# Kernel tuning notes

Measured on AMD Instinct MI355X. Metric: run time of the kernel, lower is better.

## Reference

```python
import jax, jax.numpy as jnp
import numpy as np

D_MODEL = 768
D_STATE = 16
D_CONV = 4
EXPAND = 2
N_LAYERS = 2
HEADDIM = 64
PATCH_DIM = 256
D_INNER = EXPAND * D_MODEL            # 1536
NHEADS = D_INNER // HEADDIM           # 24
CONV_DIM = D_INNER + 2 * D_STATE      # 1568 (x, B, C share the conv)
D_IN_PROJ = 2 * D_INNER + 2 * D_STATE + NHEADS  # 3128


def _mamba2(u, w_in, conv_w, conv_b, dt_bias, A_log, D, norm_w, w_out):
    """Mamba2 block (ngroups=1, rmsnorm=True, non-fused reference path)."""
    b, l, _ = u.shape
    zxbcdt = u @ w_in                                   # (b,l,D_IN_PROJ)
    z = zxbcdt[..., :D_INNER]
    xBC = zxbcdt[..., D_INNER:D_INNER + CONV_DIM]
    dt = jax.nn.softplus(zxbcdt[..., D_INNER + CONV_DIM:] + dt_bias)  # (b,l,H)
    # causal depthwise conv1d over L, then silu
    kernel = conv_w.T[:, None, :]                       # (D_CONV,1,CONV_DIM)
    xBC = jax.lax.conv_general_dilated(
        xBC, kernel, (1,), [(D_CONV - 1, 0)],
        dimension_numbers=('NLC', 'LIO', 'NLC'),
        feature_group_count=CONV_DIM) + conv_b
    xBC = jax.nn.silu(xBC)
    x = xBC[..., :D_INNER].reshape(b, l, NHEADS, HEADDIM)
    B = xBC[..., D_INNER:D_INNER + D_STATE]             # (b,l,N)
    C = xBC[..., D_INNER + D_STATE:]                    # (b,l,N)
    A = -jnp.exp(A_log)                                 # (H,)

    def step(h, inp):
        dt_t, x_t, b_t, c_t = inp                       # (b,H),(b,H,P),(b,N),(b,N)
        dA = jnp.exp(dt_t * A)                          # (b,H)
        h = h * dA[:, :, None, None] + jnp.einsum('bh,bhp,bn->bhpn', dt_t, x_t, b_t)
        y_t = jnp.einsum('bhpn,bn->bhp', h, c_t)
        return h, y_t

    h0 = jnp.zeros((b, NHEADS, HEADDIM, D_STATE), u.dtype)
    _, y = jax.lax.scan(step, h0,
                        (dt.swapaxes(0, 1), x.swapaxes(0, 1),
                         B.swapaxes(0, 1), C.swapaxes(0, 1)))
    y = y.swapaxes(0, 1) + x * D[:, None]               # skip: D per head
    y = y.reshape(b, l, D_INNER)
    # gated RMSNorm: rmsnorm(y * silu(z)) * weight
    g = y * jax.nn.silu(z)
    g = g * jax.lax.rsqrt(jnp.mean(g * g, axis=-1, keepdims=True) + 1e-5)
    y = g * norm_w
    return y @ w_out


def _backbone(patch_embeddings, Wp, bp, in_w, conv_w, conv_b, dt_bias,
              A_log, Dh, norm_w, out_w, bi_w, ls, fin_w):
    x = patch_embeddings @ Wp + bp
    for i in range(N_LAYERS):
        h_f = _mamba2(x, in_w[i, 0], conv_w[i, 0], conv_b[i, 0], dt_bias[i, 0],
                      A_log[i, 0], Dh[i, 0], norm_w[i, 0], out_w[i, 0])
        h_b = jnp.flip(_mamba2(jnp.flip(x, 1), in_w[i, 1], conv_w[i, 1],
                               conv_b[i, 1], dt_bias[i, 1], A_log[i, 1],
                               Dh[i, 1], norm_w[i, 1], out_w[i, 1]), 1)
        m = jnp.concatenate([h_f, h_b], axis=-1) @ bi_w[i]
        x = x + m * ls[i]
    # final RMSNorm with unit offset
    v = jnp.mean(x * x, axis=-1, keepdims=True)
    return x * jax.lax.rsqrt(v + 1e-6) * (1.0 + fin_w)


def setup_inputs() -> dict:
    key = jax.random.key(0)
    ks = jax.random.split(key, 14)
    L2 = (N_LAYERS, 2)
    pe = jax.random.normal(ks[0], (2, 2048, PATCH_DIM), jnp.float32)
    Wp = jax.random.normal(ks[1], (PATCH_DIM, D_MODEL), jnp.float32) * 0.02
    bp = jnp.zeros((D_MODEL,), jnp.float32)
    in_w = jax.random.normal(ks[2], L2 + (D_MODEL, D_IN_PROJ), jnp.float32) * 0.02
    conv_w = jax.random.normal(ks[3], L2 + (CONV_DIM, D_CONV), jnp.float32) * 0.2
    conv_b = jnp.zeros(L2 + (CONV_DIM,), jnp.float32)
    dt_bias = jax.random.uniform(ks[4], L2 + (NHEADS,), jnp.float32, -4.0, -2.0)
    A_log = jnp.log(jax.random.uniform(ks[5], L2 + (NHEADS,), jnp.float32, 1.0, 16.0))
    Dh = jax.random.normal(ks[6], L2 + (NHEADS,), jnp.float32) * 0.1 + 1.0
    norm_w = jnp.ones(L2 + (D_INNER,), jnp.float32)
    out_w = jax.random.normal(ks[7], L2 + (D_INNER, D_MODEL), jnp.float32) * 0.02
    bi_w = jax.random.normal(ks[8], (N_LAYERS, 2 * D_MODEL, D_MODEL), jnp.float32) * 0.02
    ls = jnp.full((N_LAYERS, D_MODEL), 1e-4, jnp.float32)
    fin_w = jnp.zeros((D_MODEL,), jnp.float32)
    return {"patch_embeddings": pe, "Wp": Wp, "bp": bp, "in_w": in_w,
            "conv_w": conv_w, "conv_b": conv_b, "dt_bias": dt_bias,
            "A_log": A_log, "Dh": Dh, "norm_w": norm_w, "out_w": out_w,
            "bi_w": bi_w, "ls": ls, "fin_w": fin_w}


def reference(patch_embeddings, Wp, bp, in_w, conv_w, conv_b, dt_bias,
              A_log, Dh, norm_w, out_w, bi_w, ls, fin_w):
    return _backbone(patch_embeddings, Wp, bp, in_w, conv_w, conv_b, dt_bias,
                     A_log, Dh, norm_w, out_w, bi_w, ls, fin_w)
```

## Files before the change

### kernel.cpp

```cpp
#include <hip/hip_runtime.h>

typedef unsigned short u16;
typedef short s16x8 __attribute__((ext_vector_type(8)));
typedef u16 u16x8 __attribute__((ext_vector_type(8)));
typedef float f32x4 __attribute__((ext_vector_type(4)));

__device__ inline float bf2f(u16 u) {
    union { unsigned int i; float f; } w; w.i = ((unsigned int)u) << 16; return w.f;
}
__device__ inline u16 f2bf(float f) {
    union { float f; unsigned int i; } w; w.f = f;
    unsigned int u = w.i;
    u += 0x7fffu + ((u >> 16) & 1u);
    return (u16)(u >> 16);
}

__global__ __launch_bounds__(256)
void wtransT(const float* __restrict__ src, u16* __restrict__ dst,
             int K, int N, int dstride, int src_z, int dz_hi, int dz_lo)
{
    int z = blockIdx.z;
    src += (size_t)z * src_z;
    dst += (size_t)(z >> 1) * dz_hi + (size_t)(z & 1) * dz_lo;
    __shared__ float t[32][33];
    int kt = blockIdx.y * 32, nt0 = blockIdx.x * 32;
    int lx = threadIdx.x & 31, ly = threadIdx.x >> 5;
#pragma unroll
    for (int i = 0; i < 32; i += 8) {
        int k = kt + ly + i, n = nt0 + lx;
        t[ly + i][lx] = (k < K && n < N) ? src[(size_t)k * N + n] : 0.f;
    }
    __syncthreads();
#pragma unroll
    for (int i = 0; i < 32; i += 8) {
        int n = nt0 + ly + i, k = kt + lx;
        if (n < N && k < K) dst[(size_t)n * dstride + k] = f2bf(t[lx][ly + i]);
    }
}

__global__ void cvtk(const float* __restrict__ src, u16* __restrict__ dst, int n) {
    int i = blockIdx.x * 256 + threadIdx.x;
    if (i < n) dst[i] = f2bf(src[i]);
}

__global__ __launch_bounds__(256, 2)
void gemm8(const u16* __restrict__ A, const u16* __restrict__ WT,
           int M, int N, int K,
           u16* __restrict__ bout, int ostride)
{
    __shared__ u16 lds8[2 * 16384];

    int mt, nt;
    {
        int nwg = gridDim.x * gridDim.y;
        int f = blockIdx.y * gridDim.x + blockIdx.x;
        int q = nwg >> 3, r = nwg & 7;
        int xcd = f & 7, lo = f >> 3;
        int wid = (xcd < r ? xcd * (q + 1) : r * (q + 1) + (xcd - r) * q) + lo;
        mt = wid % gridDim.y; nt = wid / gridDim.y;
    }

    const int tid  = threadIdx.x;
    const int lane = tid & 63;
    const int wave = tid >> 6;
    const int wm = wave >> 1, wn = wave & 1;
    const int r16 = lane & 15;
    const int lg  = lane >> 4;
    const int mb  = mt * 128;
    const int nb  = nt * 128;
    const int wbase = tid & 192;

    f32x4 acc[4][4];
#pragma unroll
    for (int mi = 0; mi < 4; mi++)
#pragma unroll
        for (int ni = 0; ni < 4; ni++)
            acc[mi][ni] = (f32x4){0.f, 0.f, 0.f, 0.f};

    auto stage = [&](int buf, int k0) {
        u16* bA = &lds8[buf * 16384];
        u16* bB = bA + 8192;
#pragma unroll
        for (int r = 0; r < 4; r++) {
            int e = r * 256 + tid;
            int row = e >> 3;
            int cbs = (e & 7) ^ (row & 7);
            const u16* g = A + (size_t)(mb + row) * K + k0 + cbs * 8;
            __builtin_amdgcn_global_load_lds(
                (const __attribute__((address_space(1))) void*)g,
                (__attribute__((address_space(3))) void*)&bA[(r * 256 + wbase) * 8],
                16, 0, 0);
        }
#pragma unroll
        for (int r = 0; r < 4; r++) {
            int e = r * 256 + tid;
            int row = e >> 3;
            int cbs = (e & 7) ^ (row & 7);
            const u16* g = WT + (size_t)(nb + row) * K + k0 + cbs * 8;
            __builtin_amdgcn_global_load_lds(
                (const __attribute__((address_space(1))) void*)g,
                (__attribute__((address_space(3))) void*)&bB[(r * 256 + wbase) * 8],
                16, 0, 0);
        }
    };

    const int ntk = K >> 6;
    stage(0, 0);
    stage(1, 64);
    asm volatile("s_waitcnt vmcnt(8)" ::: "memory");
    __builtin_amdgcn_sched_barrier(0);
    __builtin_amdgcn_s_barrier();

    for (int t = 0; t < ntk; t++) {
        const int buf = t & 1;
        const u16* bA = &lds8[buf * 16384];
        const u16* bB = bA + 8192;
        s16x8 a[4][2], b[4][2];
#pragma unroll
        for (int mf = 0; mf < 4; mf++)
#pragma unroll
            for (int kk = 0; kk < 2; kk++) {
                int row = wm * 64 + mf * 16 + r16;
                int cb = (kk * 4 + lg) ^ (row & 7);
                a[mf][kk] = *(const s16x8*)&bA[row * 64 + cb * 8];
            }
#pragma unroll
        for (int nf = 0; nf < 4; nf++)
#pragma unroll
            for (int kk = 0; kk < 2; kk++) {
                int row = wn * 64 + nf * 16 + r16;
                int cb = (kk * 4 + lg) ^ (row & 7);
                b[nf][kk] = *(const s16x8*)&bB[row * 64 + cb * 8];
            }
        asm volatile("s_waitcnt lgkmcnt(0)" ::: "memory");
        __builtin_amdgcn_sched_barrier(0);
        __builtin_amdgcn_s_barrier();
        if (t + 2 < ntk) {
            stage(buf, (t + 2) << 6);
            asm volatile("s_waitcnt vmcnt(8)" ::: "memory");
        } else {
            asm volatile("s_waitcnt vmcnt(0)" ::: "memory");
        }
        __builtin_amdgcn_sched_barrier(0);
        __builtin_amdgcn_s_barrier();
        __builtin_amdgcn_s_setprio(1);
#pragma unroll
        for (int mf = 0; mf < 4; mf++)
#pragma unroll
            for (int nf = 0; nf < 4; nf++) {
                acc[mf][nf] = __builtin_amdgcn_mfma_f32_16x16x32_bf16(
                    a[mf][0], b[nf][0], acc[mf][nf], 0, 0, 0);
                acc[mf][nf] = __builtin_amdgcn_mfma_f32_16x16x32_bf16(
                    a[mf][1], b[nf][1], acc[mf][nf], 0, 0, 0);
            }
        __builtin_amdgcn_s_setprio(0);
    }

#pragma unroll
    for (int mf = 0; mf < 4; mf++) {
        const int rowb = mb + wm * 64 + mf * 16 + lg * 4;
#pragma unroll
        for (int nf = 0; nf < 4; nf++) {
            int col = nb + wn * 64 + nf * 16 + r16;
            if (col < N) {
#pragma unroll
                for (int j = 0; j < 4; j++)
                    bout[(size_t)(rowb + j) * ostride + col] = f2bf(acc[mf][nf][j]);
            }
        }
    }
}

template<int BM, int BN, int EPI>
__global__ __launch_bounds__(256)
void gemmL(const u16* __restrict__ A, const u16* __restrict__ WT,
           int M, int N, int K,
           float* __restrict__ fout, u16* __restrict__ bout,
           const float* __restrict__ bias, const float* __restrict__ lsv,
           int ostride, int ocoloff,
           size_t aZ, size_t wZ, size_t oZ, int ocolZ)
{
    constexpr int MI = BM / 32, NI = BN / 32;
    constexpr int BUF = (BM + BN) * 32;
    constexpr int RA = BM / 64, RB = BN / 64;
    __shared__ u16 lds[2 * BUF];

    {
        int z = blockIdx.z;
        A += (size_t)z * aZ; WT += (size_t)z * wZ;
        bout += (size_t)(z >> 1) * oZ; ocoloff += (z & 1) * ocolZ;
    }

    int mt, nt;
    {
        int nwg = gridDim.x * gridDim.y;
        int f = blockIdx.y * gridDim.x + blockIdx.x;
        int q = nwg >> 3, r = nwg & 7;
        int xcd = f & 7, lo = f >> 3;
        int wid = (xcd < r ? xcd * (q + 1) : r * (q + 1) + (xcd - r) * q) + lo;
        mt = wid % gridDim.y; nt = wid / gridDim.y;
    }

    const int tid  = threadIdx.x;
    const int lane = tid & 63;
    const int wave = tid >> 6;
    const int wm = wave >> 1, wn = wave & 1;
    const int r16 = lane & 15;
    const int ks  = (lane >> 4) * 8;
    const int mb  = mt * BM;
    const int nb  = nt * BN;
    const int wbase = tid & 192;

    f32x4 acc[MI][NI];
#pragma unroll
    for (int mi = 0; mi < MI; mi++)
#pragma unroll
        for (int ni = 0; ni < NI; ni++)
            acc[mi][ni] = (f32x4){0.f, 0.f, 0.f, 0.f};

    auto stage = [&](int buf, int k0) {
        u16* bufA = &lds[buf * BUF];
        u16* bufB = &lds[buf * BUF + BM * 32];
#pragma unroll
        for (int r = 0; r < RA; r++) {
            int c = r * 256 + tid;
            const u16* g = A + (size_t)(mb + (c >> 2)) * K + k0 + (c & 3) * 8;
            __builtin_amdgcn_global_load_lds(
                (const __attribute__((address_space(1))) void*)g,
                (__attribute__((address_space(3))) void*)&bufA[(r * 256 + wbase) * 8],
                16, 0, 0);
        }
#pragma unroll
        for (int r = 0; r < RB; r++) {
            int c = r * 256 + tid;
            const u16* g = WT + (size_t)(nb + (c >> 2)) * K + k0 + (c & 3) * 8;
            __builtin_amdgcn_global_load_lds(
                (const __attribute__((address_space(1))) void*)g,
                (__attribute__((address_space(3))) void*)&bufB[(r * 256 + wbase) * 8],
                16, 0, 0);
        }
    };
    auto compute = [&](int buf) {
        const u16* bufA = &lds[buf * BUF];
        const u16* bufB = &lds[buf * BUF + BM * 32];
        s16x8 af[MI], bfr[NI];
#pragma unroll
        for (int mi = 0; mi < MI; mi++)
            af[mi] = *(const s16x8*)&bufA[(wm * (BM / 2) + mi * 16 + r16) * 32 + ks];
#pragma unroll
        for (int ni = 0; ni < NI; ni++)
            bfr[ni] = *(const s16x8*)&bufB[(wn * (BN / 2) + ni * 16 + r16) * 32 + ks];
#pragma unroll
        for (int mi = 0; mi < MI; mi++)
#pragma unroll
            for (int ni = 0; ni < NI; ni++)
                acc[mi][ni] = __builtin_amdgcn_mfma_f32_16x16x32_bf16(
                    af[mi], bfr[ni], acc[mi][ni], 0, 0, 0);
    };

    const int nt2 = K >> 5;
    stage(0, 0);
    __syncthreads();
    for (int t = 0; t < nt2; t++) {
        if (t + 1 < nt2) stage((t + 1) & 1, (t + 1) << 5);
        compute(t & 1);
        __syncthreads();
    }

#pragma unroll
    for (int mi = 0; mi < MI; mi++) {
        const int rowb = mb + wm * (BM / 2) + mi * 16 + (lane >> 4) * 4;
#pragma unroll
        for (int ni = 0; ni < NI; ni++) {
            int col = nb + wn * (BN / 2) + ni * 16 + r16;
            if (col < N) {
#pragma unroll
                for (int j = 0; j < 4; j++) {
                    int row = rowb + j;
                    float v = acc[mi][ni][j];
                    if (EPI == 0) {
                        v += bias[col];
                        size_t o = (size_t)row * ostride + col;
                        fout[o] = v; bout[o] = f2bf(v);
                    } else if (EPI == 1) {
                        bout[(size_t)row * ostride + ocoloff + col] = f2bf(v);
                    } else {
                        size_t o = (size_t)row * 768 + col;
                        float xv = fout[o] + v * lsv[col];
                        fout[o] = xv; bout[o] = f2bf(xv);
                    }
                }
            }
        }
    }
}

__global__ void dtk(const u16* __restrict__ zxAll, float* __restrict__ dtAll,
                    const float* __restrict__ dtb)
{
    int idx = blockIdx.x * 256 + threadIdx.x;
    if (idx >= 2 * 4096 * 24) return;
    int dir = idx / (4096 * 24);
    int r   = idx % (4096 * 24);
    int row = r / 24, h = r % 24;
    float raw = bf2f(zxAll[(size_t)row * 6256 + dir * 3128 + 3104 + h]) + dtb[dir * 24 + h];
    dtAll[((size_t)dir * 4096 + row) * 24 + h] = raw > 20.f ? raw : log1pf(__expf(raw));
}

__global__ __launch_bounds__(256)
void scan1k(const u16* __restrict__ zxAll, const float* __restrict__ dtAll,
            const float* __restrict__ cw, const float* __restrict__ cb,
            const float* __restrict__ Alog, const float* __restrict__ Dhp,
            u16* __restrict__ yAll, float* __restrict__ states, float* __restrict__ decays)
{
    const int c   = blockIdx.x;
    const int bh  = blockIdx.y;
    const int dir = blockIdx.z;
    const int b = bh / 24, h = bh % 24;
    const float* dtp = dtAll + (size_t)dir * 4096 * 24;
    u16* yp = yAll + dir * 1536;
    const float Av = -__expf(Alog[dir * 24 + h]);
    const float Dv = Dhp[dir * 24 + h];
    const int inst = (dir * 2 + b) * 24 + h;

    const int tid  = threadIdx.x;
    const int lane = tid & 63;
    const int wave = tid >> 6;
    const int r16  = lane & 15;
    const int ks   = (lane >> 4) * 8;

    __shared__ u16 xT[64][72];
    __shared__ u16 Gs[64][72];
    __shared__ u16 Bs[64][40];
    __shared__ u16 Cs[64][40];
    __shared__ u16 SBT[16][72];
    __shared__ float dts[64], cds[64];

    const u16* zxd = zxAll + dir * 3128 + 1536;
    auto growp = [&](int ii) -> const u16* {
        int l = dir ? (2047 - ii) : ii;
        return zxd + ((size_t)b * 2048 + l) * 6256;
    };
    auto rowof = [&](int t) -> size_t {
        int i = c * 64 + t;
        int l = dir ? (2047 - i) : i;
        return (size_t)b * 2048 + l;
    };
    const u16x8 zz = {0,0,0,0,0,0,0,0};

    {
        int tr = tid >> 2, pg = tid & 3;
        int chb = h * 64 + pg * 16;
        int i0 = c * 64 + tr;
        u16x8 tv[4][2];
#pragma unroll
        for (int k = 0; k < 4; k++) {
            int ii = i0 - 3 + k;
            if (ii >= 0) {
                const u16* s = growp(ii) + chb;
                tv[k][0] = *(const u16x8*)s;
                tv[k][1] = *(const u16x8*)(s + 8);
            } else { tv[k][0] = zz; tv[k][1] = zz; }
        }
        const float* cwp = cw + ((size_t)dir * 1568 + chb) * 4;
        const float* cbp = cb + (size_t)dir * 1568 + chb;
#pragma unroll
        for (int j = 0; j < 16; j++) {
            f32x4 wj = *(const f32x4*)(cwp + j * 4);
            float a = cbp[j];
            int hi = j >> 3, lo2 = j & 7;
            a += bf2f(tv[0][hi][lo2]) * wj[0] + bf2f(tv[1][hi][lo2]) * wj[1]
               + bf2f(tv[2][hi][lo2]) * wj[2] + bf2f(tv[3][hi][lo2]) * wj[3];
            a = a / (1.f + __expf(-a));
            xT[pg * 16 + j][tr] = f2bf(a);
        }
    }
    {
        int t = tid & 63, which = tid >> 6;
        if (which < 2) {
            int chb = 1536 + which * 16;
            int i0 = c * 64 + t;
            u16x8 tv[4][2];
#pragma unroll
            for (int k = 0; k < 4; k++) {
                int ii = i0 - 3 + k;
                if (ii >= 0) {
                    const u16* s = growp(ii) + chb;
                    tv[k][0] = *(const u16x8*)s;
                    tv[k][1] = *(const u16x8*)(s + 8);
                } else { tv[k][0] = zz; tv[k][1] = zz; }
            }
            const float* cwp = cw + ((size_t)dir * 1568 + chb) * 4;
            const float* cbp = cb + (size_t)dir * 1568 + chb;
            u16* dst = which ? &Cs[t][0] : &Bs[t][0];
#pragma unroll
            for (int j = 0; j < 16; j++) {
                f32x4 wj = *(const f32x4*)(cwp + j * 4);
                float a = cbp[j];
                int hi = j >> 3, lo2 = j & 7;
                a += bf2f(tv[0][hi][lo2]) * wj[0] + bf2f(tv[1][hi][lo2]) * wj[1]
                   + bf2f(tv[2][hi][lo2]) * wj[2] + bf2f(tv[3][hi][lo2]) * wj[3];
                a = a / (1.f + __expf(-a));
                dst[j] = f2bf(a);
            }
        } else {
            u16* dst = (which == 2) ? &Bs[t][16] : &Cs[t][16];
            *(u16x8*)dst = zz; *(u16x8*)(dst + 8) = zz;
        }
    }
    if (tid < 64) {
        float v = dtp[rowof(tid) * 24 + h];
        dts[tid] = v;
        float s = v;
#pragma unroll
        for (int o = 1; o < 64; o <<= 1) {
            float nvl = __shfl_up(s, o, 64);
            if (lane >= o) s += nvl;
        }
        cds[tid] = s;
    }
    __syncthreads();

    {
        const s16x8 af = *(const s16x8*)&Cs[wave * 16 + r16][ks];
#pragma unroll
        for (int st = 0; st < 4; st++) {
            const s16x8 bfr = *(const s16x8*)&Bs[st * 16 + r16][ks];
            f32x4 a2 = {0.f, 0.f, 0.f, 0.f};
            a2 = __builtin_amdgcn_mfma_f32_16x16x32_bf16(af, bfr, a2, 0, 0, 0);
            int s = st * 16 + (lane & 15);
            int tbase = wave * 16 + (lane >> 4) * 4;
            float cs = cds[s], dtv = dts[s];
#pragma unroll
            for (int j = 0; j < 4; j++) {
                int t = tbase + j;
                float g = 0.f;
                if (s <= t) {
                    g = a2[j] * dtv * __expf(Av * (cds[t] - cs));
                    if (s == t) g += Dv;
                }
                Gs[t][s] = f2bf(g);
            }
        }
    }
    {
        float cdT = cds[63];
        int s = tid & 63;
        float sc = __expf(Av * (cdT - cds[s])) * dts[s];
#pragma unroll
        for (int it = 0; it < 4; it++) {
            int n = (tid >> 6) + it * 4;
            SBT[n][s] = f2bf(sc * bf2f(Bs[s][n]));
        }
    }
    __syncthreads();

    {
#pragma unroll
        for (int pt = 0; pt < 4; pt++) {
            f32x4 a2 = {0.f, 0.f, 0.f, 0.f};
#pragma unroll
            for (int kk = 0; kk < 2; kk++) {
                s16x8 af = *(const s16x8*)&Gs[wave * 16 + r16][kk * 32 + ks];
                s16x8 bfr = *(const s16x8*)&xT[pt * 16 + r16][kk * 32 + ks];
                a2 = __builtin_amdgcn_mfma_f32_16x16x32_bf16(af, bfr, a2, 0, 0, 0);
            }
            int p = pt * 16 + (lane & 15);
            int tbase = wave * 16 + (lane >> 4) * 4;
#pragma unroll
            for (int j = 0; j < 4; j++) {
                size_t row = rowof(tbase + j);
                yp[row * 3072 + h * 64 + p] = f2bf(a2[j]);
            }
        }
    }
    {
        f32x4 a2 = {0.f, 0.f, 0.f, 0.f};
#pragma unroll
        for (int kk = 0; kk < 2; kk++) {
            s16x8 af = *(const s16x8*)&xT[wave * 16 + r16][kk * 32 + ks];
            s16x8 bfr = *(const s16x8*)&SBT[r16][kk * 32 + ks];
            a2 = __builtin_amdgcn_mfma_f32_16x16x32_bf16(af, bfr, a2, 0, 0, 0);
        }
        int n = lane & 15;
        int pbase = wave * 16 + (lane >> 4) * 4;
        float* st = states + ((size_t)inst * 32 + c) * 1024;
#pragma unroll
        for (int j = 0; j < 4; j++) st[(pbase + j) * 16 + n] = a2[j];
        if (tid == 0) decays[inst * 32 + c] = __expf(Av * cds[63]);
    }
}

__global__ __launch_bounds__(256)
void scan2k(float* __restrict__ states, const float* __restrict__ decays)
{
    int inst = blockIdx.x;
    int tid = threadIdx.x;
    float* base = states + (size_t)inst * 32 * 1024 + tid * 4;
    const float* dec = decays + inst * 32;
    f32x4 hreg = {0.f, 0.f, 0.f, 0.f};
    f32x4 L = *(f32x4*)base;
    for (int cc = 0; cc < 32; cc++) {
        f32x4 Lnext;
        if (cc + 1 < 32) Lnext = *(f32x4*)(base + (cc + 1) * 1024);
        *(f32x4*)(base + cc * 1024) = hreg;
        float d = dec[cc];
        hreg = hreg * d + L;
        L = Lnext;
    }
}

__global__ __launch_bounds__(256)
void scan3k(const float* __restrict__ states,
            const u16* __restrict__ zxAll, const float* __restrict__ dtAll,
            const float* __restrict__ cw, const float* __restrict__ cb,
            const float* __restrict__ Alog, u16* __restrict__ yAll)
{
    const int c   = blockIdx.x + 1;
    const int bh  = blockIdx.y;
    const int dir = blockIdx.z;
    const int b = bh / 24, h = bh % 24;
    const float* dtp = dtAll + (size_t)dir * 4096 * 24;
    u16* yp = yAll + dir * 1536;
    const float Av = -__expf(Alog[dir * 24 + h]);
    const int inst = (dir * 2 + b) * 24 + h;
    const int tid = threadIdx.x;

    __shared__ float hs[64][20];
    __shared__ u16 Cs3[64][16];
    __shared__ float ets[64];

    const u16* zxd = zxAll + dir * 3128 + 1536;
    auto growp = [&](int ii) -> const u16* {
        int l = dir ? (2047 - ii) : ii;
        return zxd + ((size_t)b * 2048 + l) * 6256;
    };
    auto rowof = [&](int t) -> size_t {
        int i = c * 64 + t;
        int l = dir ? (2047 - i) : i;
        return (size_t)b * 2048 + l;
    };

    {
        const float* sp = states + ((size_t)inst * 32 + c) * 1024 + tid * 4;
        f32x4 v = *(const f32x4*)sp;
        int e = tid * 4;
        int p = e >> 4, n = e & 15;
        hs[p][n] = v[0]; hs[p][n+1] = v[1]; hs[p][n+2] = v[2]; hs[p][n+3] = v[3];
    }
    if (tid < 64) {
        int i0 = c * 64 + tid;
        u16x8 tv[4][2];
#pragma unroll
        for (int k = 0; k < 4; k++) {
            const u16* s = growp(i0 - 3 + k) + 1552;
            tv[k][0] = *(const u16x8*)s;
            tv[k][1] = *(const u16x8*)(s + 8);
        }
        const float* cwp = cw + ((size_t)dir * 1568 + 1552) * 4;
        const float* cbp = cb + (size_t)dir * 1568 + 1552;
#pragma unroll
        for (int j = 0; j < 16; j++) {
            f32x4 wj = *(const f32x4*)(cwp + j * 4);
            float a = cbp[j];
            int hi = j >> 3, lo2 = j & 7;
            a += bf2f(tv[0][hi][lo2]) * wj[0] + bf2f(tv[1][hi][lo2]) * wj[1]
               + bf2f(tv[2][hi][lo2]) * wj[2] + bf2f(tv[3][hi][lo2]) * wj[3];
            a = a / (1.f + __expf(-a));
            Cs3[tid][j] = f2bf(a);
        }
        float v = dtp[rowof(tid) * 24 + h];
        float s = v;
#pragma unroll
        for (int o = 1; o < 64; o <<= 1) {
            float nvl = __shfl_up(s, o, 64);
            if ((tid & 63) >= o) s += nvl;
        }
        ets[tid] = __expf(Av * s);
    }
    __syncthreads();

    int t = tid >> 2, pg = tid & 3;
    float cv[16];
    float et = ets[t];
#pragma unroll
    for (int n = 0; n < 16; n++) cv[n] = bf2f(Cs3[t][n]) * et;
    size_t row = rowof(t);
    u16* yrow = yp + row * 3072 + h * 64 + pg * 16;
    u16x8 ya = *(u16x8*)yrow;
    u16x8 yb = *(u16x8*)(yrow + 8);
#pragma unroll
    for (int jj = 0; jj < 16; jj++) {
        int p = pg * 16 + jj;
        float acc = 0.f;
#pragma unroll
        for (int q = 0; q < 4; q++) {
            f32x4 hv = *(const f32x4*)&hs[p][q * 4];
            acc += cv[q*4]*hv[0] + cv[q*4+1]*hv[1] + cv[q*4+2]*hv[2] + cv[q*4+3]*hv[3];
        }
        if (jj < 8) ya[jj] = f2bf(bf2f(ya[jj]) + acc);
        else        yb[jj - 8] = f2bf(bf2f(yb[jj - 8]) + acc);
    }
    *(u16x8*)yrow = ya;
    *(u16x8*)(yrow + 8) = yb;
}

__global__ __launch_bounds__(256)
void gatek(const u16* __restrict__ zxAll, u16* __restrict__ yAll,
           const float* __restrict__ nw)
{
    int row = blockIdx.x, dir = blockIdx.y;
    const u16* zx = zxAll + (size_t)row * 6256 + dir * 3128;
    u16* y = yAll + (size_t)row * 3072 + dir * 1536;
    const float* nwp = nw + dir * 1536;
    int tid = threadIdx.x;
    float g[6]; float s = 0.f;
#pragma unroll
    for (int j = 0; j < 6; j++) {
        int c = j * 256 + tid;
        float z  = bf2f(zx[c]);
        float yv = bf2f(y[c]);
        float gv = yv * z / (1.f + __expf(-z));
        g[j] = gv; s += gv * gv;
    }
    __shared__ float red[4];
    for (int o = 32; o; o >>= 1) s += __shfl_down(s, o, 64);
    if ((tid & 63) == 0) red[tid >> 6] = s;
    __syncthreads();
    s = red[0] + red[1] + red[2] + red[3];
    float sc = rsqrtf(s * (1.f / 1536.f) + 1e-5f);
#pragma unroll
    for (int j = 0; j < 6; j++) {
        int c = j * 256 + tid;
        y[c] = f2bf(g[j] * sc * nwp[c]);
    }
}

__global__ __launch_bounds__(256)
void finalk(const float* __restrict__ x, const float* __restrict__ fw, float* __restrict__ out)
{
    int row = blockIdx.x; int tid = threadIdx.x;
    const float* xr = x + (size_t)row * 768;
    float v[3]; float s = 0.f;
#pragma unroll
    for (int j = 0; j < 3; j++) {
        int c = j * 256 + tid;
        v[j] = xr[c]; s += v[j] * v[j];
    }
    __shared__ float red[4];
    for (int o = 32; o; o >>= 1) s += __shfl_down(s, o, 64);
    if ((tid & 63) == 0) red[tid >> 6] = s;
    __syncthreads();
    s = red[0] + red[1] + red[2] + red[3];
    float sc = rsqrtf(s * (1.f / 768.f) + 1e-6f);
#pragma unroll
    for (int j = 0; j < 3; j++) {
        int c = j * 256 + tid;
        out[(size_t)row * 768 + c] = v[j] * sc * (1.f + fw[c]);
    }
}

extern "C" void kernel_launch(void* const* d_in, const int* in_sizes, int n_in,
                              void* d_out, int out_size, void* d_ws, size_t ws_size,
                              hipStream_t stream)
{
    const float* pe      = (const float*)d_in[0];
    const float* Wp      = (const float*)d_in[1];
    const float* bp      = (const float*)d_in[2];
    const float* in_w    = (const float*)d_in[3];
    const float* conv_w  = (const float*)d_in[4];
    const float* conv_b  = (const float*)d_in[5];
    const float* dt_bias = (const float*)d_in[6];
    const float* A_log   = (const float*)d_in[7];
    const float* Dh      = (const float*)d_in[8];
    const float* norm_w  = (const float*)d_in[9];
    const float* out_w   = (const float*)d_in[10];
    const float* bi_w    = (const float*)d_in[11];
    const float* ls      = (const float*)d_in[12];
    const float* fin_w   = (const float*)d_in[13];

    char* wp = (char*)d_ws;
    auto alloc = [&](size_t bytes) {
        char* r = wp; wp += (bytes + 255) & ~(size_t)255; return r;
    };
    u16*   WpT    = (u16*)  alloc((size_t)768 * 256 * 2);
    u16*   inWT   = (u16*)  alloc((size_t)2 * 6272 * 768 * 2);
    u16*   outWB  = (u16*)  alloc((size_t)4 * 1536 * 768 * 2);
    u16*   biWT   = (u16*)  alloc((size_t)4 * 768 * 768 * 2);
    u16*   WcombT = (u16*)  alloc((size_t)2 * 768 * 3072 * 2);
    u16*   peB    = (u16*)  alloc((size_t)4096 * 256 * 2);
    float* x      = (float*)alloc((size_t)4096 * 768 * 4);
    u16*   xb     = (u16*)  alloc((size_t)4096 * 768 * 2);
    u16*   zxAll  = (u16*)  alloc((size_t)4096 * 6256 * 2);
    float* dtAll  = (float*)alloc((size_t)2 * 4096 * 24 * 4);
    u16*   yAll   = (u16*)  alloc((size_t)4096 * 3072 * 2);
    float* states = (float*)alloc((size_t)96 * 32 * 1024 * 4);
    float* decays = (float*)alloc((size_t)96 * 32 * 4);

    wtransT<<<dim3(24, 8, 1), 256, 0, stream>>>(Wp, WpT, 256, 768, 256, 0, 0, 0);
    wtransT<<<dim3(98, 24, 4), 256, 0, stream>>>(in_w, inWT, 768, 3128, 768,
                                                 2402304, 4816896, 2402304);
    wtransT<<<dim3(24, 24, 4), 256, 0, stream>>>(bi_w, biWT, 768, 768, 768,
                                                 589824, 1179648, 589824);
    cvtk<<<(4 * 1536 * 768 + 255) / 256, 256, 0, stream>>>(out_w, outWB, 4 * 1536 * 768);
    cvtk<<<4096, 256, 0, stream>>>(pe, peB, 4096 * 256);

    gemmL<64, 64, 1><<<dim3(24, 12, 4), 256, 0, stream>>>(
        biWT, outWB, 768, 1536, 768, nullptr, WcombT,
        nullptr, nullptr, 3072, 0,
        (size_t)589824, (size_t)1179648, (size_t)768 * 3072, 1536);

    gemmL<64, 64, 0><<<dim3(12, 64, 1), 256, 0, stream>>>(
        peB, WpT, 4096, 768, 256, x, xb, bp, nullptr, 768, 0, 0, 0, 0, 0);

    for (int i = 0; i < 2; i++) {
        gemm8<<<dim3(49, 32, 1), 256, 0, stream>>>(
            xb, inWT + (size_t)i * 6272 * 768, 4096, 6256, 768, zxAll, 6256);
        dtk<<<(2 * 4096 * 24 + 255) / 256, 256, 0, stream>>>(zxAll, dtAll, dt_bias + i * 48);
        scan1k<<<dim3(32, 48, 2), 256, 0, stream>>>(zxAll, dtAll,
                                                    conv_w + (size_t)i * 2 * 1568 * 4,
                                                    conv_b + (size_t)i * 2 * 1568,
                                                    A_log + i * 48, Dh + i * 48,
                                                    yAll, states, decays);
        scan2k<<<96, 256, 0, stream>>>(states, decays);
        scan3k<<<dim3(31, 48, 2), 256, 0, stream>>>(states, zxAll, dtAll,
                                                    conv_w + (size_t)i * 2 * 1568 * 4,
                                                    conv_b + (size_t)i * 2 * 1568,
                                                    A_log + i * 48, yAll);
        gatek<<<dim3(4096, 2), 256, 0, stream>>>(zxAll, yAll, norm_w + (size_t)i * 2 * 1536);
        gemmL<128, 64, 2><<<dim3(12, 32, 1), 256, 0, stream>>>(
            yAll, WcombT + (size_t)i * 768 * 3072, 4096, 768, 3072,
            x, xb, nullptr, ls + i * 768, 768, 0, 0, 0, 0, 0);
    }

    finalk<<<4096, 256, 0, stream>>>(x, fin_w, (float*)d_out);
}
```

Before: 489.3 us.

## Generalize pipelined GEMM, fuse dt softplus into in-proj epilogue, reuse for out-proj

Measured after the change: 493.5 us. Within noise of the previous version (+0.9%).

```diff
diff --git a/kernel.cpp b/kernel.cpp
--- a/kernel.cpp
+++ b/kernel.cpp
@@ -43,21 +43,33 @@
     if (i < n) dst[i] = f2bf(src[i]);
 }
 
+template<int BM, int BN, int SM, int EPI>
 __global__ __launch_bounds__(256, 2)
-void gemm8(const u16* __restrict__ A, const u16* __restrict__ WT,
+void gemmP(const u16* __restrict__ A, const u16* __restrict__ WT,
            int M, int N, int K,
-           u16* __restrict__ bout, int ostride)
-{
-    __shared__ u16 lds8[2 * 16384];
+           float* __restrict__ fout, u16* __restrict__ bout,
+           const float* __restrict__ aux, float* __restrict__ dtAll,
+           int ostride)
+{
+    constexpr int MI = BM / 32;
+    constexpr int NI = BN / 32;
+    constexpr int L  = (BM + BN) / 32;
+    constexpr int TBUF = (BM + BN) * 64;
+    __shared__ u16 lds8[2 * TBUF];
 
     int mt, nt;
     {
-        int nwg = gridDim.x * gridDim.y;
-        int f = blockIdx.y * gridDim.x + blockIdx.x;
+        int NT = gridDim.x, MT = gridDim.y;
+        int nwg = NT * MT;
+        int f = blockIdx.y * NT + blockIdx.x;
         int q = nwg >> 3, r = nwg & 7;
         int xcd = f & 7, lo = f >> 3;
         int wid = (xcd < r ? xcd * (q + 1) : r * (q + 1) + (xcd - r) * q) + lo;
-        mt = wid % gridDim.y; nt = wid / gridDim.y;
+        int band = wid / (SM * NT);
+        int pos  = wid % (SM * NT);
+        nt = pos / SM;
+        mt = band * SM + pos % SM;
+        (void)MT;
     }
 
     const int tid  = threadIdx.x;
@@ -66,40 +78,30 @@
     const int wm = wave >> 1, wn = wave & 1;
     const int r16 = lane & 15;
     const int lg  = lane >> 4;
-    const int mb  = mt * 128;
-    const int nb  = nt * 128;
+    const int mb  = mt * BM;
+    const int nb  = nt * BN;
     const int wbase = tid & 192;
 
-    f32x4 acc[4][4];
-#pragma unroll
-    for (int mi = 0; mi < 4; mi++)
-#pragma unroll
-        for (int ni = 0; ni < 4; ni++)
+    f32x4 acc[MI][NI];
+#pragma unroll
+    for (int mi = 0; mi < MI; mi++)
+#pragma unroll
+        for (int ni = 0; ni < NI; ni++)
             acc[mi][ni] = (f32x4){0.f, 0.f, 0.f, 0.f};
 
     auto stage = [&](int buf, int k0) {
-        u16* bA = &lds8[buf * 16384];
-        u16* bB = bA + 8192;
-#pragma unroll
-        for (int r = 0; r < 4; r++) {
-            int e = r * 256 + tid;
+        u16* bA = &lds8[buf * TBUF];
+#pragma unroll
+        for (int rr = 0; rr < L; rr++) {
+            int e = rr * 256 + tid;
             int row = e >> 3;
             int cbs = (e & 7) ^ (row & 7);
-            const u16* g = A + (size_t)(mb + row) * K + k0 + cbs * 8;
+            const u16* g = (rr < BM / 32)
+                ? A  + (size_t)(mb + row) * K + k0 + cbs * 8
+                : WT + (size_t)(nb + row - BM) * K + k0 + cbs * 8;
             __builtin_amdgcn_global_load_lds(
                 (const __attribute__((address_space(1))) void*)g,
-                (__attribute__((address_space(3))) void*)&bA[(r * 256 + wbase) * 8],
-                16, 0, 0);
-        }
-#pragma unroll
-        for (int r = 0; r < 4; r++) {
-            int e = r * 256 + tid;
-            int row = e >> 3;
-            int cbs = (e & 7) ^ (row & 7);
-            const u16* g = WT + (size_t)(nb + row) * K + k0 + cbs * 8;
-            __builtin_amdgcn_global_load_lds(
-                (const __attribute__((address_space(1))) void*)g,
-                (__attribute__((address_space(3))) void*)&bB[(r * 256 + wbase) * 8],
+                (__attribute__((address_space(3))) void*)&bA[(rr * 256 + wbase) * 8],
                 16, 0, 0);
         }
     };
@@ -107,37 +109,55 @@
     const int ntk = K >> 6;
     stage(0, 0);
     stage(1, 64);
-    asm volatile("s_waitcnt vmcnt(8)" ::: "memory");
+    if constexpr (L == 8) asm volatile("s_waitcnt vmcnt(8)" ::: "memory");
+    else                  asm volatile("s_waitcnt vmcnt(6)" ::: "memory");
     __builtin_amdgcn_sched_barrier(0);
     __builtin_amdgcn_s_barrier();
 
     for (int t = 0; t < ntk; t++) {
         const int buf = t & 1;
-        const u16* bA = &lds8[buf * 16384];
-        const u16* bB = bA + 8192;
-        s16x8 a[4][2], b[4][2];
-#pragma unroll
-        for (int mf = 0; mf < 4; mf++)
-#pragma unroll
-            for (int kk = 0; kk < 2; kk++) {
-                int row = wm * 64 + mf * 16 + r16;
-                int cb = (kk * 4 + lg) ^ (row & 7);
-                a[mf][kk] = *(const s16x8*)&bA[row * 64 + cb * 8];
-            }
-#pragma unroll
-        for (int nf = 0; nf < 4; nf++)
-#pragma unroll
-            for (int kk = 0; kk < 2; kk++) {
-                int row = wn * 64 + nf * 16 + r16;
-                int cb = (kk * 4 + lg) ^ (row & 7);
-                b[nf][kk] = *(const s16x8*)&bB[row * 64 + cb * 8];
-            }
+        const u16* bA = &lds8[buf * TBUF];
+        const u16* bB = bA + BM * 64;
+        s16x8 a0[MI], b0[NI], a1[MI], b1[NI];
+#pragma unroll
+        for (int mf = 0; mf < MI; mf++) {
+            int row = wm * (BM / 2) + mf * 16 + r16;
+            a0[mf] = *(const s16x8*)&bA[row * 64 + (lg ^ (row & 7)) * 8];
+        }
+#pragma unroll
+        for (int nf = 0; nf < NI; nf++) {
+            int row = wn * (BN / 2) + nf * 16 + r16;
+            b0[nf] = *(const s16x8*)&bB[row * 64 + (lg ^ (row & 7)) * 8];
+        }
+        __builtin_amdgcn_sched_barrier(0);
+#pragma unroll
+        for (int mf = 0; mf < MI; mf++) {
+            int row = wm * (BM / 2) + mf * 16 + r16;
+            a1[mf] = *(const s16x8*)&bA[row * 64 + ((4 + lg) ^ (row & 7)) * 8];
+        }
+#pragma unroll
+        for (int nf = 0; nf < NI; nf++) {
+            int row = wn * (BN / 2) + nf * 16 + r16;
+            b1[nf] = *(const s16x8*)&bB[row * 64 + ((4 + lg) ^ (row & 7)) * 8];
+        }
+        if constexpr (MI + NI == 8) asm volatile("s_waitcnt lgkmcnt(8)" ::: "memory");
+        else                        asm volatile("s_waitcnt lgkmcnt(6)" ::: "memory");
+        __builtin_amdgcn_sched_barrier(0);
+        __builtin_amdgcn_s_setprio(1);
+#pragma unroll
+        for (int mf = 0; mf < MI; mf++)
+#pragma unroll
+            for (int nf = 0; nf < NI; nf++)
+                acc[mf][nf] = __builtin_amdgcn_mfma_f32_16x16x32_bf16(
+                    a0[mf], b0[nf], acc[mf][nf], 0, 0, 0);
+        __builtin_amdgcn_s_setprio(0);
         asm volatile("s_waitcnt lgkmcnt(0)" ::: "memory");
         __builtin_amdgcn_sched_barrier(0);
         __builtin_amdgcn_s_barrier();
         if (t + 2 < ntk) {
             stage(buf, (t + 2) << 6);
-            asm volatile("s_waitcnt vmcnt(8)" ::: "memory");
+            if constexpr (L == 8) asm volatile("s_waitcnt vmcnt(8)" ::: "memory");
+            else                  asm volatile("s_waitcnt vmcnt(6)" ::: "memory");
         } else {
             asm volatile("s_waitcnt vmcnt(0)" ::: "memory");
         }
@@ -145,27 +165,41 @@
         __builtin_amdgcn_s_barrier();
         __builtin_amdgcn_s_setprio(1);
 #pragma unroll
-        for (int mf = 0; mf < 4; mf++)
-#pragma unroll
-            for (int nf = 0; nf < 4; nf++) {
+        for (int mf = 0; mf < MI; mf++)
+#pragma unroll
+            for (int nf = 0; nf < NI; nf++)
                 acc[mf][nf] = __builtin_amdgcn_mfma_f32_16x16x32_bf16(
-                    a[mf][0], b[nf][0], acc[mf][nf], 0, 0, 0);
-                acc[mf][nf] = __builtin_amdgcn_mfma_f32_16x16x32_bf16(
-                    a[mf][1], b[nf][1], acc[mf][nf], 0, 0, 0);
-            }
+                    a1[mf], b1[nf], acc[mf][nf], 0, 0, 0);
         __builtin_amdgcn_s_setprio(0);
     }
 
 #pragma unroll
-    for (int mf = 0; mf < 4; mf++) {
-        const int rowb = mb + wm * 64 + mf * 16 + lg * 4;
-#pragma unroll
-        for (int nf = 0; nf < 4; nf++) {
-            int col = nb + wn * 64 + nf * 16 + r16;
+    for (int mf = 0; mf < MI; mf++) {
+        const int rowb = mb + wm * (BM / 2) + mf * 16 + lg * 4;
+#pragma unroll
+        for (int nf = 0; nf < NI; nf++) {
+            int col = nb + wn * (BN / 2) + nf * 16 + r16;
             if (col < N) {
 #pragma unroll
-                for (int j = 0; j < 4; j++)
-                    bout[(size_t)(rowb + j) * ostride + col] = f2bf(acc[mf][nf][j]);
+                for (int j = 0; j < 4; j++) {
+                    int row = rowb + j;
+                    float v = acc[mf][nf][j];
+                    if (EPI == 2) {
+                        size_t o = (size_t)row * 768 + col;
+                        float xv = fout[o] + v * aux[col];
+                        fout[o] = xv; bout[o] = f2bf(xv);
+                    } else {
+                        bout[(size_t)row * ostride + col] = f2bf(v);
+                        int dirc = col >= 3128;
+                        int cc = col - dirc * 3128;
+                        if (cc >= 3104) {
+                            int hh = cc - 3104;
+                            float raw = v + aux[dirc * 24 + hh];
+                            float dtv = raw > 20.f ? raw : log1pf(__expf(raw));
+                            dtAll[((size_t)dirc * 4096 + row) * 24 + hh] = dtv;
+                        }
+                    }
+                }
             }
         }
     }
@@ -293,18 +327,6 @@
             }
         }
     }
-}
-
-__global__ void dtk(const u16* __restrict__ zxAll, float* __restrict__ dtAll,
-                    const float* __restrict__ dtb)
-{
-    int idx = blockIdx.x * 256 + threadIdx.x;
-    if (idx >= 2 * 4096 * 24) return;
-    int dir = idx / (4096 * 24);
-    int r   = idx % (4096 * 24);
-    int row = r / 24, h = r % 24;
-    float raw = bf2f(zxAll[(size_t)row * 6256 + dir * 3128 + 3104 + h]) + dtb[dir * 24 + h];
-    dtAll[((size_t)dir * 4096 + row) * 24 + h] = raw > 20.f ? raw : log1pf(__expf(raw));
 }
 
 __global__ __launch_bounds__(256)
@@ -714,9 +736,9 @@
         peB, WpT, 4096, 768, 256, x, xb, bp, nullptr, 768, 0, 0, 0, 0, 0);
 
     for (int i = 0; i < 2; i++) {
-        gemm8<<<dim3(49, 32, 1), 256, 0, stream>>>(
-            xb, inWT + (size_t)i * 6272 * 768, 4096, 6256, 768, zxAll, 6256);
-        dtk<<<(2 * 4096 * 24 + 255) / 256, 256, 0, stream>>>(zxAll, dtAll, dt_bias + i * 48);
+        gemmP<128, 128, 8, 3><<<dim3(49, 32), 256, 0, stream>>>(
+            xb, inWT + (size_t)i * 6272 * 768, 4096, 6256, 768,
+            nullptr, zxAll, dt_bias + i * 48, dtAll, 6256);
         scan1k<<<dim3(32, 48, 2), 256, 0, stream>>>(zxAll, dtAll,
                                                     conv_w + (size_t)i * 2 * 1568 * 4,
                                                     conv_b + (size_t)i * 2 * 1568,
@@ -728,9 +750,9 @@
                                                     conv_b + (size_t)i * 2 * 1568,
                                                     A_log + i * 48, yAll);
         gatek<<<dim3(4096, 2), 256, 0, stream>>>(zxAll, yAll, norm_w + (size_t)i * 2 * 1536);
-        gemmL<128, 64, 2><<<dim3(12, 32, 1), 256, 0, stream>>>(
+        gemmP<128, 64, 4, 2><<<dim3(12, 32), 256, 0, stream>>>(
             yAll, WcombT + (size_t)i * 768 * 3072, 4096, 768, 3072,
-            x, xb, nullptr, ls + i * 768, 768, 0, 0, 0, 0, 0);
+            x, xb, ls + i * 768, nullptr, 768);
     }
 
     finalk<<<4096, 256, 0, stream>>>(x, fin_w, (float*)d_out);
```

## Add specialized output-projection GEMM with direct-to-LDS loads and XCD-aware tile mapping

Applied to the files above, without the earlier changes.

Result: no change. 498.3 us (+1.8%).

```diff
diff --git a/kernel.cpp b/kernel.cpp
--- a/kernel.cpp
+++ b/kernel.cpp
@@ -166,6 +166,125 @@
 #pragma unroll
                 for (int j = 0; j < 4; j++)
                     bout[(size_t)(rowb + j) * ostride + col] = f2bf(acc[mf][nf][j]);
+            }
+        }
+    }
+}
+
+__global__ __launch_bounds__(256, 2)
+void gemm9(const u16* __restrict__ A, const u16* __restrict__ WT, int K,
+           float* __restrict__ fout, u16* __restrict__ bout,
+           const float* __restrict__ lsv)
+{
+    __shared__ u16 lds9[2 * 12288];
+
+    int mt, nt;
+    {
+        int nwg = gridDim.x * gridDim.y;
+        int f = blockIdx.y * gridDim.x + blockIdx.x;
+        int q = nwg >> 3, r = nwg & 7;
+        int xcd = f & 7, lo = f >> 3;
+        int wid = (xcd < r ? xcd * (q + 1) : r * (q + 1) + (xcd - r) * q) + lo;
+        mt = wid % gridDim.y; nt = wid / gridDim.y;
+    }
+
+    const int tid  = threadIdx.x;
+    const int lane = tid & 63;
+    const int wave = tid >> 6;
+    const int wm = wave >> 1, wn = wave & 1;
+    const int r16 = lane & 15;
+    const int lg  = lane >> 4;
+    const int mb  = mt * 128;
+    const int nb  = nt * 64;
+    const int wbase = tid & 192;
+
+    f32x4 acc[4][2];
+#pragma unroll
+    for (int mi = 0; mi < 4; mi++)
+#pragma unroll
+        for (int ni = 0; ni < 2; ni++)
+            acc[mi][ni] = (f32x4){0.f, 0.f, 0.f, 0.f};
+
+    auto stage = [&](int buf, int k0) {
+        u16* bA = &lds9[buf * 12288];
+#pragma unroll
+        for (int rr = 0; rr < 6; rr++) {
+            int e = rr * 256 + tid;
+            int row = e >> 3;
+            int cbs = (e & 7) ^ (row & 7);
+            const u16* g = (rr < 4)
+                ? A  + (size_t)(mb + row) * K + k0 + cbs * 8
+                : WT + (size_t)(nb + row - 128) * K + k0 + cbs * 8;
+            __builtin_amdgcn_global_load_lds(
+                (const __attribute__((address_space(1))) void*)g,
+                (__attribute__((address_space(3))) void*)&bA[(rr * 256 + wbase) * 8],
+                16, 0, 0);
+        }
+    };
+
+    const int ntk = K >> 6;
+    stage(0, 0);
+    stage(1, 64);
+    asm volatile("s_waitcnt vmcnt(6)" ::: "memory");
+    __builtin_amdgcn_sched_barrier(0);
+    __builtin_amdgcn_s_barrier();
+
+    for (int t = 0; t < ntk; t++) {
+        const int buf = t & 1;
+        const u16* bA = &lds9[buf * 12288];
+        const u16* bB = bA + 8192;
+        s16x8 a[4][2], b[2][2];
+#pragma unroll
+        for (int mf = 0; mf < 4; mf++)
+#pragma unroll
+            for (int kk = 0; kk < 2; kk++) {
+                int row = wm * 64 + mf * 16 + r16;
+                int cb = (kk * 4 + lg) ^ (row & 7);
+                a[mf][kk] = *(const s16x8*)&bA[row * 64 + cb * 8];
+            }
+#pragma unroll
+        for (int nf = 0; nf < 2; nf++)
+#pragma unroll
+            for (int kk = 0; kk < 2; kk++) {
+                int row = wn * 32 + nf * 16 + r16;
+                int cb = (kk * 4 + lg) ^ (row & 7);
+                b[nf][kk] = *(const s16x8*)&bB[row * 64 + cb * 8];
+            }
+        asm volatile("s_waitcnt lgkmcnt(0)" ::: "memory");
+        __builtin_amdgcn_sched_barrier(0);
+        __builtin_amdgcn_s_barrier();
+        if (t + 2 < ntk) {
+            stage(buf, (t + 2) << 6);
+            asm volatile("s_waitcnt vmcnt(6)" ::: "memory");
+        } else {
+            asm volatile("s_waitcnt vmcnt(0)" ::: "memory");
+        }
+        __builtin_amdgcn_sched_barrier(0);
+        __builtin_amdgcn_s_barrier();
+        __builtin_amdgcn_s_setprio(1);
+#pragma unroll
+        for (int mf = 0; mf < 4; mf++)
+#pragma unroll
+            for (int nf = 0; nf < 2; nf++) {
+                acc[mf][nf] = __builtin_amdgcn_mfma_f32_16x16x32_bf16(
+                    a[mf][0], b[nf][0], acc[mf][nf], 0, 0, 0);
+                acc[mf][nf] = __builtin_amdgcn_mfma_f32_16x16x32_bf16(
+                    a[mf][1], b[nf][1], acc[mf][nf], 0, 0, 0);
+            }
+        __builtin_amdgcn_s_setprio(0);
+    }
+
+#pragma unroll
+    for (int mf = 0; mf < 4; mf++) {
+        const int rowb = mb + wm * 64 + mf * 16 + lg * 4;
+#pragma unroll
+        for (int nf = 0; nf < 2; nf++) {
+            int col = nb + wn * 32 + nf * 16 + r16;
+#pragma unroll
+            for (int j = 0; j < 4; j++) {
+                size_t o = (size_t)(rowb + j) * 768 + col;
+                float xv = fout[o] + acc[mf][nf][j] * lsv[col];
+                fout[o] = xv; bout[o] = f2bf(xv);
             }
         }
     }
@@ -728,9 +847,8 @@
                                                     conv_b + (size_t)i * 2 * 1568,
                                                     A_log + i * 48, yAll);
         gatek<<<dim3(4096, 2), 256, 0, stream>>>(zxAll, yAll, norm_w + (size_t)i * 2 * 1536);
-        gemmL<128, 64, 2><<<dim3(12, 32, 1), 256, 0, stream>>>(
-            yAll, WcombT + (size_t)i * 768 * 3072, 4096, 768, 3072,
-            x, xb, nullptr, ls + i * 768, 768, 0, 0, 0, 0, 0);
+        gemm9<<<dim3(12, 32, 1), 256, 0, stream>>>(
+            yAll, WcombT + (size_t)i * 768 * 3072, 3072, x, xb, ls + i * 768);
     }
 
     finalk<<<4096, 256, 0, stream>>>(x, fin_w, (float*)d_out);
```
